# Performance work log

Measured on AMD Instinct MI355X. Metric: run time of the kernel, lower is better.

The kernel has to match this reference:

```python
import jax, jax.numpy as jnp
import numpy as np

EPS = 1e-6
LN3 = 1.0986122886681098  # ternary_softmax uses base-3 exponentials: 3**x / sum(3**x)
ROPE_BASE = 10000.0


def exact_rmsnorm(x, g):
    # ExactRMSNorm: x / sqrt(mean(x^2) + eps) * g
    ms = jnp.mean(jnp.square(x), axis=-1, keepdims=True)
    return x * jax.lax.rsqrt(ms + EPS) * g


def ternary_rope(t):
    # Rotary embedding whose cos/sin tables are quantized to {-1, 0, +1}
    # (round() of cos/sin in [-1,1] yields exactly the ternary set).
    S, D = t.shape[-2], t.shape[-1]
    half = D // 2
    inv_freq = 1.0 / (ROPE_BASE ** (jnp.arange(half, dtype=jnp.float32) / half))
    ang = jnp.arange(S, dtype=jnp.float32)[:, None] * inv_freq[None, :]  # [S, half]
    cos = jnp.round(jnp.cos(ang))
    sin = jnp.round(jnp.sin(ang))
    cos = jnp.concatenate([cos, cos], axis=-1)  # [S, D]
    sin = jnp.concatenate([sin, sin], axis=-1)
    rot = jnp.concatenate([-t[..., half:], t[..., :half]], axis=-1)
    return t * cos + rot * sin


def ternary_softmax(x, axis=-1):
    # softmax in base 3: 3**x / sum(3**x) == softmax(x * ln 3)
    return jax.nn.softmax(x * LN3, axis=axis)


def setup_inputs() -> dict:
    key = jax.random.key(0)
    ks = jax.random.split(key, 6)
    B, S, D = 4, 4096, 1024
    x = jax.random.normal(ks[0], (B, S, D), dtype=jnp.float32)
    g_norm = jnp.ones((D,), dtype=jnp.float32)
    w_qkv = jax.random.normal(ks[1], (D, 3 * D), dtype=jnp.float32) * 0.02
    b_qkv = jnp.zeros((3 * D,), dtype=jnp.float32)
    w_proj = jax.random.normal(ks[2], (D, D), dtype=jnp.float32) * 0.02
    b_proj = jnp.zeros((D,), dtype=jnp.float32)
    return {"x": x, "g_norm": g_norm, "w_qkv": w_qkv, "b_qkv": b_qkv,
            "w_proj": w_proj, "b_proj": b_proj}


def reference(x, g_norm, w_qkv, b_qkv, w_proj, b_proj):
    D = x.shape[-1]
    scale = 1.0 / jnp.sqrt(jnp.float32(D))
    residual = x
    h = exact_rmsnorm(x, g_norm)
    qkv = h @ w_qkv + b_qkv  # [B, S, 3D]
    q, k, v = jnp.split(qkv, 3, axis=-1)
    q = ternary_rope(q)
    k = ternary_rope(k)
    scores = jnp.einsum("bsd,btd->bst", q, k) * scale  # [B, S, S]
    attn = ternary_softmax(scores, axis=-1)
    o = jnp.einsum("bst,btd->bsd", attn, v)
    return o @ w_proj + b_proj + residual
```

## Files before the change

### kernel.cpp

```cpp
#include <hip/hip_runtime.h>
#include <hip/hip_fp8.h>
#include <stdint.h>

#define DEVI __device__ __forceinline__

typedef unsigned short u16;
typedef uint8_t u8;
typedef __attribute__((ext_vector_type(8))) __bf16 bf16x8;
typedef __attribute__((ext_vector_type(4))) float f32x4;
typedef __attribute__((ext_vector_type(4))) int i32x4;
typedef __attribute__((ext_vector_type(8))) int i32x8;

DEVI float b2f(u16 u) { union { unsigned int i; float f; } v; v.i = ((unsigned int)u) << 16; return v.f; }
DEVI u16 f2b(float f) {
  union { float f; unsigned int i; } v; v.f = f;
  unsigned int r = v.i + 0x7fffu + ((v.i >> 16) & 1u);
  return (u16)(r >> 16);
}
DEVI u8 f2f8(float f) { __hip_fp8_e4m3 t(f); return t.__x; }

DEVI void gld_lds16(const void* g, void* l) {
  __builtin_amdgcn_global_load_lds((const __attribute__((address_space(1))) unsigned int*)g,
                                   (__attribute__((address_space(3))) unsigned int*)l, 16, 0, 0);
}

DEVI i32x8 ld32(const u8* p0, const u8* p1) {
  i32x4 lo = *(const i32x4*)p0;
  i32x4 hi = *(const i32x4*)p1;
  return __builtin_shufflevector(lo, hi, 0, 1, 2, 3, 4, 5, 6, 7);
}


__global__ __launch_bounds__(256) void k_rmsnorm(const float* __restrict__ x,
                                                 const float* __restrict__ g,
                                                 u8* __restrict__ h) {
  const int row = blockIdx.x;
  const int t = threadIdx.x;
  const float4 v = ((const float4*)(x + (size_t)row * 1024))[t];
  float ss = v.x * v.x + v.y * v.y + v.z * v.z + v.w * v.w;
  for (int off = 32; off > 0; off >>= 1) ss += __shfl_down(ss, off);
  __shared__ float red[4];
  if ((t & 63) == 0) red[t >> 6] = ss;
  __syncthreads();
  const float tot = red[0] + red[1] + red[2] + red[3];
  const float sc = rsqrtf(tot * (1.0f / 1024.0f) + 1e-6f);
  const float4 gv = ((const float4*)g)[t];
  uchar4 o;
  o.x = f2f8(v.x * sc * gv.x); o.y = f2f8(v.y * sc * gv.y);
  o.z = f2f8(v.z * sc * gv.z); o.w = f2f8(v.w * sc * gv.w);
  *(uchar4*)(h + (size_t)row * 1024 + t * 4) = o;
}

__global__ __launch_bounds__(256) void k_transpose_cast(const float* __restrict__ src,
                                                        int rows, int cols,
                                                        u16* __restrict__ dst) {
  __shared__ float tile[32][33];
  const int c0 = blockIdx.x * 32, r0 = blockIdx.y * 32;
  const int tx = threadIdx.x, ty = threadIdx.y;
  for (int i = 0; i < 32; i += 8)
    tile[ty + i][tx] = src[(size_t)(r0 + ty + i) * cols + c0 + tx];
  __syncthreads();
  for (int i = 0; i < 32; i += 8)
    dst[(size_t)(c0 + ty + i) * rows + r0 + tx] = f2b(tile[tx][ty + i]);
}

__global__ __launch_bounds__(256) void k_transpose_cast_f8(const float* __restrict__ src,
                                                           int rows, int cols,
                                                           u8* __restrict__ dst) {
  __shared__ float tile[32][33];
  const int c0 = blockIdx.x * 32, r0 = blockIdx.y * 32;
  const int tx = threadIdx.x, ty = threadIdx.y;
  for (int i = 0; i < 32; i += 8)
    tile[ty + i][tx] = src[(size_t)(r0 + ty + i) * cols + c0 + tx];
  __syncthreads();
  for (int i = 0; i < 32; i += 8)
    dst[(size_t)(c0 + ty + i) * rows + r0 + tx] = f2f8(tile[tx][ty + i] * 32.0f);
}

__global__ __launch_bounds__(256) void k_rope_cast(const u16* __restrict__ q16, const u16* __restrict__ k16,
                                                   u8* __restrict__ q8, u8* __restrict__ k8) {
  const int row = blockIdx.x;
  const int pos = row & 4095;
  const int t = threadIdx.x;
  const int j0 = t * 2;
  float c[2], s[2];
#pragma unroll
  for (int u = 0; u < 2; u++) {
    const float e = (float)(j0 + u) * (1.0f / 512.0f);
    const float invf = exp2f(-13.287712379549449f * e);
    const float ang = (float)pos * invf;
    c[u] = rintf(cosf(ang));
    s[u] = rintf(sinf(ang));
  }
  const u16* qr = q16 + (size_t)row * 1024;
  const u16* kr = k16 + (size_t)row * 1024;
  u8* qo = q8 + (size_t)row * 1024;
  u8* ko = k8 + (size_t)row * 1024;
  const ushort2 qa = *(const ushort2*)(qr + j0), qb = *(const ushort2*)(qr + j0 + 512);
  const ushort2 ka = *(const ushort2*)(kr + j0), kb = *(const ushort2*)(kr + j0 + 512);
  uchar2 o;
  o.x = f2f8(b2f(qa.x) * c[0] - b2f(qb.x) * s[0]);
  o.y = f2f8(b2f(qa.y) * c[1] - b2f(qb.y) * s[1]);
  *(uchar2*)(qo + j0) = o;
  o.x = f2f8(b2f(qb.x) * c[0] + b2f(qa.x) * s[0]);
  o.y = f2f8(b2f(qb.y) * c[1] + b2f(qa.y) * s[1]);
  *(uchar2*)(qo + j0 + 512) = o;
  o.x = f2f8(b2f(ka.x) * c[0] - b2f(kb.x) * s[0]);
  o.y = f2f8(b2f(ka.y) * c[1] - b2f(kb.y) * s[1]);
  *(uchar2*)(ko + j0) = o;
  o.x = f2f8(b2f(kb.x) * c[0] + b2f(ka.x) * s[0]);
  o.y = f2f8(b2f(kb.y) * c[1] + b2f(ka.y) * s[1]);
  *(uchar2*)(ko + j0 + 512) = o;
}

__global__ __launch_bounds__(256) void k_vt(const u16* __restrict__ v, u8* __restrict__ vt) {
  __shared__ u16 tile[32][33];
  const int b = blockIdx.z;
  const int s0 = blockIdx.x * 32, d0 = blockIdx.y * 32;
  const int tx = threadIdx.x, ty = threadIdx.y;
  for (int i = 0; i < 32; i += 8)
    tile[ty + i][tx] = v[(size_t)(b * 4096 + s0 + ty + i) * 1024 + d0 + tx];
  __syncthreads();
  for (int i = 0; i < 32; i += 8)
    vt[(size_t)(b * 1024 + d0 + ty + i) * 4096 + s0 + tx] = f2f8(b2f(tile[tx][ty + i]));
}

DEVI void gemm_tile(const u16* __restrict__ A, int lda,
                    const u16* __restrict__ B, int ldb,
                    int K, int m0, int n0,
                    u16* As, u16* Bs, f32x4 acc[4][4]) {
  const int t = threadIdx.x;
  const int sr = t >> 2;
  const int sc = (t & 3) * 8;
  const u16* Ag0 = A + (size_t)(m0 + sr) * lda + sc;
  const u16* Ag1 = A + (size_t)(m0 + 64 + sr) * lda + sc;
  const u16* Bg0 = B + (size_t)(n0 + sr) * ldb + sc;
  const u16* Bg1 = B + (size_t)(n0 + 64 + sr) * ldb + sc;
  u16* Asw = As + t * 8;
  u16* Bsw = Bs + t * 8;

  const int lane = t & 63, qd = lane >> 4, l16 = lane & 15;
  const int wave = t >> 6;
  const int wm = (wave >> 1) * 64, wn = (wave & 1) * 64;
  const int aoff = (wm + l16) * 32 + qd * 8;
  const int boff = (wn + l16) * 32 + qd * 8;

  auto stage = [&](int sel, int k0) {
    u16* Ad = Asw + sel * 4096;
    u16* Bd = Bsw + sel * 4096;
    gld_lds16(Ag0 + k0, Ad);
    gld_lds16(Ag1 + k0, Ad + 2048);
    gld_lds16(Bg0 + k0, Bd);
    gld_lds16(Bg1 + k0, Bd + 2048);
  };

  stage(0, 0);
  int cur = 0;
  for (int k0 = 0; k0 < K; k0 += 32) {
    if (k0 + 32 < K) {
      stage(cur ^ 1, k0 + 32);
      asm volatile("s_waitcnt vmcnt(4)" ::: "memory");
    } else {
      asm volatile("s_waitcnt vmcnt(0)" ::: "memory");
    }
    __builtin_amdgcn_s_barrier();
    const u16* Ard = As + cur * 4096 + aoff;
    const u16* Brd = Bs + cur * 4096 + boff;
    bf16x8 af[4], bfv[4];
#pragma unroll
    for (int i = 0; i < 4; i++) af[i] = *(const bf16x8*)(Ard + i * 16 * 32);
#pragma unroll
    for (int j = 0; j < 4; j++) bfv[j] = *(const bf16x8*)(Brd + j * 16 * 32);
#pragma unroll
    for (int i = 0; i < 4; i++)
#pragma unroll
      for (int j = 0; j < 4; j++)
        acc[i][j] = __builtin_amdgcn_mfma_f32_16x16x32_bf16(af[i], bfv[j], acc[i][j], 0, 0, 0);
    __builtin_amdgcn_s_barrier();
    cur ^= 1;
  }
}

DEVI void gemm_tile_mx(const u8* __restrict__ A, int lda,
                       const u8* __restrict__ B, int ldb,
                       int K, int m0, int n0,
                       u8* As, u8* Bs, f32x4 acc[4][4], int sB) {
  const int t = threadIdx.x;
  const int sr = t >> 3;
  const int sc = ((t & 7) ^ (sr & 7)) << 4;
  const u8* Agb = A + (size_t)(m0 + sr) * lda + sc;
  const u8* Bgb = B + (size_t)(n0 + sr) * ldb + sc;
  u8* Asw = As + t * 16;
  u8* Bsw = Bs + t * 16;

  const int lane = t & 63, qd = lane >> 4, l16 = lane & 15;
  const int wave = t >> 6;
  const int wm = (wave >> 1) * 64, wn = (wave & 1) * 64;
  const int key = l16 & 7;
  const int c0 = ((qd << 1) ^ key) << 4;
  const int aoff = (wm + l16) * 128 + c0;
  const int boff = (wn + l16) * 128 + c0;

  auto stage = [&](int sel, int k0) {
    u8* Ad = Asw + sel * 16384;
    u8* Bd = Bsw + sel * 16384;
#pragma unroll
    for (int l = 0; l < 4; l++) {
      gld_lds16(Agb + k0 + (size_t)l * 32 * lda, Ad + l * 4096);
      gld_lds16(Bgb + k0 + (size_t)l * 32 * ldb, Bd + l * 4096);
    }
  };

  stage(0, 0);
  int cur = 0;
  for (int k0 = 0; k0 < K; k0 += 128) {
    if (k0 + 128 < K) {
      stage(cur ^ 1, k0 + 128);
      asm volatile("s_waitcnt vmcnt(8)" ::: "memory");
    } else {
      asm volatile("s_waitcnt vmcnt(0)" ::: "memory");
    }
    __builtin_amdgcn_s_barrier();
    const u8* Ab = As + cur * 16384;
    const u8* Bb = Bs + cur * 16384;
    i32x8 a[4], b[4];
#pragma unroll
    for (int i = 0; i < 4; i++)
      a[i] = ld32(Ab + aoff + i * 2048, Ab + (aoff ^ 16) + i * 2048);
#pragma unroll
    for (int j = 0; j < 4; j++)
      b[j] = ld32(Bb + boff + j * 2048, Bb + (boff ^ 16) + j * 2048);
#pragma unroll
    for (int i = 0; i < 4; i++)
#pragma unroll
      for (int j = 0; j < 4; j++)
        acc[i][j] = __builtin_amdgcn_mfma_scale_f32_16x16x128_f8f6f4(
            a[i], b[j], acc[i][j], 0 , 0 ,
            0, 0x7f7f7f7f, 0, sB);
    __builtin_amdgcn_s_barrier();
    cur ^= 1;
  }
}

#define ACC_INIT()                                               \
  f32x4 acc[4][4];                                               \
  _Pragma("unroll") for (int i = 0; i < 4; i++)                  \
      _Pragma("unroll") for (int j = 0; j < 4; j++)              \
          acc[i][j] = f32x4{0.f, 0.f, 0.f, 0.f};

#define GEMM_EPI_IDX()                                           \
  const int t = threadIdx.x, lane = t & 63, qd = lane >> 4,      \
            l16 = lane & 15, wave = t >> 6;                      \
  const int wm = (wave >> 1) * 64, wn = (wave & 1) * 64;         \
  (void)t;


__global__ __launch_bounds__(256) void k_gemm_qkv(const u8* __restrict__ A, const u8* __restrict__ Bt,
                                                  const float* __restrict__ bias,
                                                  u16* __restrict__ q16, u16* __restrict__ k16,
                                                  u16* __restrict__ v16) {
  __shared__ alignas(16) u8 As[32768], Bs[32768];
  ACC_INIT();
  const int m0 = blockIdx.y * 128, n0 = blockIdx.x * 128;
  gemm_tile_mx(A, 1024, Bt, 1024, 1024, m0, n0, As, Bs, acc, 0x7a7a7a7a);
  GEMM_EPI_IDX();
  const int sec = n0 >> 10;
  u16* dst = (sec == 0) ? q16 : (sec == 1) ? k16 : v16;
  const int nb0 = n0 & 1023;
#pragma unroll
  for (int i = 0; i < 4; i++) {
    const int mb = m0 + wm + i * 16 + qd * 4;
#pragma unroll
    for (int j = 0; j < 4; j++) {
      const int col = n0 + wn + j * 16 + l16;
      const float bv = bias[col];
      const int dcol = nb0 + wn + j * 16 + l16;
#pragma unroll
      for (int r = 0; r < 4; r++)
        dst[(size_t)(mb + r) * 1024 + dcol] = f2b(acc[i][j][r] + bv);
    }
  }
}

__global__ __launch_bounds__(256) void k_gemm_scores(const u8* __restrict__ q, const u8* __restrict__ kk,
                                                     u8* __restrict__ P, float* __restrict__ ls) {
  __shared__ alignas(16) u8 As[32768], Bs[32768];
  ACC_INIT();
  const int b = blockIdx.z;
  const u8* A = q + (size_t)b * 4096 * 1024;
  const u8* Bt = kk + (size_t)b * 4096 * 1024;
  const int bid = blockIdx.y * 32 + blockIdx.x;
  const int xcd = bid & 7, idx = bid >> 3;
  const int m0 = ((xcd >> 2) * 16 + (idx & 15)) * 128;
  const int n0 = ((xcd & 3) * 8 + (idx >> 4)) * 128;
  gemm_tile_mx(A, 1024, Bt, 1024, 1024, m0, n0, As, Bs, acc, 0x7f7f7f7f);
  GEMM_EPI_IDX();
  const float C3 = 0.04953007814753613f;
  const size_t Pb = (size_t)b * 4096 * 4096;
  f32x4 rowp[4];
#pragma unroll
  for (int i = 0; i < 4; i++) rowp[i] = f32x4{0.f, 0.f, 0.f, 0.f};
#pragma unroll
  for (int i = 0; i < 4; i++) {
    const int mb = m0 + wm + i * 16 + qd * 4;
#pragma unroll
    for (int j = 0; j < 4; j++) {
      const int col = n0 + wn + j * 16 + l16;
#pragma unroll
      for (int r = 0; r < 4; r++) {
        const float pv = __builtin_amdgcn_exp2f(acc[i][j][r] * C3);
        P[Pb + (size_t)(mb + r) * 4096 + col] = f2f8(pv);
        rowp[i][r] += pv;
      }
    }
  }
#pragma unroll
  for (int m = 1; m < 16; m <<= 1)
#pragma unroll
    for (int i = 0; i < 4; i++) {
      rowp[i].x += __shfl_xor(rowp[i].x, m);
      rowp[i].y += __shfl_xor(rowp[i].y, m);
      rowp[i].z += __shfl_xor(rowp[i].z, m);
      rowp[i].w += __shfl_xor(rowp[i].w, m);
    }
  if (l16 == 0) {
#pragma unroll
    for (int i = 0; i < 4; i++) {
      const int mb = m0 + wm + i * 16 + qd * 4;
#pragma unroll
      for (int r = 0; r < 4; r++)
        atomicAdd(ls + (size_t)b * 4096 + mb + r, rowp[i][r]);
    }
  }
}

__global__ __launch_bounds__(256) void k_gemm_pv(const u8* __restrict__ P, const u8* __restrict__ vt,
                                                 const float* __restrict__ ls, u16* __restrict__ o) {
  __shared__ alignas(16) u8 As[32768], Bs[32768];
  ACC_INIT();
  const int b = blockIdx.z;
  const u8* A = P + (size_t)b * 4096 * 4096;
  const u8* Bt = vt + (size_t)b * 1024 * 4096;
  const int bid = blockIdx.y * 8 + blockIdx.x;
  const int xcd = bid & 7, idx = bid >> 3;
  const int m0 = ((xcd >> 1) * 8 + (idx & 7)) * 128;
  const int n0 = ((xcd & 1) * 4 + (idx >> 3)) * 128;
  gemm_tile_mx(A, 4096, Bt, 4096, 4096, m0, n0, As, Bs, acc, 0x7f7f7f7f);
  GEMM_EPI_IDX();
#pragma unroll
  for (int i = 0; i < 4; i++) {
    const int mb = m0 + wm + i * 16 + qd * 4;
    f32x4 inv;
#pragma unroll
    for (int r = 0; r < 4; r++) inv[r] = 1.0f / ls[(size_t)b * 4096 + mb + r];
#pragma unroll
    for (int j = 0; j < 4; j++) {
      const int col = n0 + wn + j * 16 + l16;
#pragma unroll
      for (int r = 0; r < 4; r++)
        o[(size_t)(b * 4096 + mb + r) * 1024 + col] = f2b(acc[i][j][r] * inv[r]);
    }
  }
}

__global__ __launch_bounds__(256) void k_gemm_proj(const u16* __restrict__ A, const u16* __restrict__ Bt,
                                                   const float* __restrict__ bias, const float* __restrict__ x,
                                                   float* __restrict__ out) {
  __shared__ alignas(16) u16 As[8192], Bs[8192];
  ACC_INIT();
  const int m0 = blockIdx.y * 128, n0 = blockIdx.x * 128;
  gemm_tile(A, 1024, Bt, 1024, 1024, m0, n0, As, Bs, acc);
  GEMM_EPI_IDX();
#pragma unroll
  for (int i = 0; i < 4; i++) {
    const int mb = m0 + wm + i * 16 + qd * 4;
#pragma unroll
    for (int j = 0; j < 4; j++) {
      const int col = n0 + wn + j * 16 + l16;
      const float bv = bias[col];
#pragma unroll
      for (int r = 0; r < 4; r++) {
        const size_t idxo = (size_t)(mb + r) * 1024 + col;
        out[idxo] = acc[i][j][r] + bv + x[idxo];
      }
    }
  }
}

extern "C" void kernel_launch(void* const* d_in, const int* in_sizes, int n_in,
                              void* d_out, int out_size, void* d_ws, size_t ws_size,
                              hipStream_t stream) {
  const float* x     = (const float*)d_in[0];
  const float* g     = (const float*)d_in[1];
  const float* wqkv  = (const float*)d_in[2];
  const float* bqkv  = (const float*)d_in[3];
  const float* wproj = (const float*)d_in[4];
  const float* bproj = (const float*)d_in[5];
  float* out = (float*)d_out;

  char* wsp = (char*)d_ws;
  size_t off = 0;
  auto take = [&](size_t bytes) -> void* {
    off = (off + 255) & ~(size_t)255;
    void* r = wsp + off;
    off += bytes;
    return r;
  };
  char* hreg = (char*)take(16384ull * 1024 * 2);
  u8*  h8   = (u8*)hreg;
  u16* o16  = (u16*)hreg;
  u8*  wqT8 = (u8*)take(3072ull * 1024);
  u16* wpT  = (u16*)take(1024ull * 1024 * 2);
  u8*  q8   = (u8*)take(16384ull * 1024);
  u8*  k8   = (u8*)take(16384ull * 1024);
  u8*  vt   = (u8*)take(4ull * 1024 * 4096);
  float* ls = (float*)take(16384ull * 4);
  char* scratch = (char*)take(3ull * 16384 * 1024 * 2);
  u16* q16 = (u16*)scratch;
  u16* k16 = (u16*)(scratch + 16384ull * 1024 * 2);
  u16* v16 = (u16*)(scratch + 2ull * 16384 * 1024 * 2);
  u8*  P   = (u8*)scratch;

  k_transpose_cast_f8<<<dim3(3072 / 32, 1024 / 32), dim3(32, 8), 0, stream>>>(wqkv, 1024, 3072, wqT8);
  k_transpose_cast<<<dim3(1024 / 32, 1024 / 32), dim3(32, 8), 0, stream>>>(wproj, 1024, 1024, wpT);
  k_rmsnorm<<<16384, 256, 0, stream>>>(x, g, h8);
  k_gemm_qkv<<<dim3(24, 128), 256, 0, stream>>>(h8, wqT8, bqkv, q16, k16, v16);
  k_rope_cast<<<16384, 256, 0, stream>>>(q16, k16, q8, k8);
  k_vt<<<dim3(128, 32, 4), dim3(32, 8), 0, stream>>>(v16, vt);
  hipMemsetAsync(ls, 0, 16384 * 4, stream);
  k_gemm_scores<<<dim3(32, 32, 4), 256, 0, stream>>>(q8, k8, P, ls);
  k_gemm_pv<<<dim3(8, 32, 4), 256, 0, stream>>>(P, vt, ls, o16);
  k_gemm_proj<<<dim3(8, 128), 256, 0, stream>>>(o16, wpT, bproj, x, out);
}
```

Measured before the change: 504.1 us.

## Load FP8 GEMM A operand directly into registers, staging only B through LDS

In the MX-FP8 GEMM tile routine, the A operand is no longer staged through shared memory. Each lane now loads its own A fragment straight from global memory into registers, double-buffered in two register sets, while B keeps its double-buffered LDS staging. The loop is unrolled by two K-steps to alternate the buffers. This halves LDS usage, which may allow more workgroups per CU, and removes LDS write/read traffic for A. In exchange it adds register pressure and less-coalesced direct global loads whose A rows are shared between waves.

After: 655.0 us. 1.3x slower.

```diff
diff --git a/kernel.cpp b/kernel.cpp
--- a/kernel.cpp
+++ b/kernel.cpp
@@ -24,10 +24,11 @@
                                    (__attribute__((address_space(3))) unsigned int*)l, 16, 0, 0);
 }
 
+DEVI i32x8 cat32(i32x4 lo, i32x4 hi) {
+  return __builtin_shufflevector(lo, hi, 0, 1, 2, 3, 4, 5, 6, 7);
+}
 DEVI i32x8 ld32(const u8* p0, const u8* p1) {
-  i32x4 lo = *(const i32x4*)p0;
-  i32x4 hi = *(const i32x4*)p1;
-  return __builtin_shufflevector(lo, hi, 0, 1, 2, 3, 4, 5, 6, 7);
+  return cat32(*(const i32x4*)p0, *(const i32x4*)p1);
 }
 
 
@@ -184,13 +185,11 @@
 DEVI void gemm_tile_mx(const u8* __restrict__ A, int lda,
                        const u8* __restrict__ B, int ldb,
                        int K, int m0, int n0,
-                       u8* As, u8* Bs, f32x4 acc[4][4], int sB) {
+                       u8* Bs, f32x4 acc[4][4], int sB) {
   const int t = threadIdx.x;
   const int sr = t >> 3;
   const int sc = ((t & 7) ^ (sr & 7)) << 4;
-  const u8* Agb = A + (size_t)(m0 + sr) * lda + sc;
   const u8* Bgb = B + (size_t)(n0 + sr) * ldb + sc;
-  u8* Asw = As + t * 16;
   u8* Bsw = Bs + t * 16;
 
   const int lane = t & 63, qd = lane >> 4, l16 = lane & 15;
@@ -198,47 +197,60 @@
   const int wm = (wave >> 1) * 64, wn = (wave & 1) * 64;
   const int key = l16 & 7;
   const int c0 = ((qd << 1) ^ key) << 4;
-  const int aoff = (wm + l16) * 128 + c0;
   const int boff = (wn + l16) * 128 + c0;
 
-  auto stage = [&](int sel, int k0) {
-    u8* Ad = Asw + sel * 16384;
+  const u8* Ab = A + (size_t)(m0 + wm + l16) * lda + qd * 32;
+
+  auto stageB = [&](int sel, int k0) {
     u8* Bd = Bsw + sel * 16384;
 #pragma unroll
-    for (int l = 0; l < 4; l++) {
-      gld_lds16(Agb + k0 + (size_t)l * 32 * lda, Ad + l * 4096);
+    for (int l = 0; l < 4; l++)
       gld_lds16(Bgb + k0 + (size_t)l * 32 * ldb, Bd + l * 4096);
-    }
   };
-
-  stage(0, 0);
-  int cur = 0;
-  for (int k0 = 0; k0 < K; k0 += 128) {
-    if (k0 + 128 < K) {
-      stage(cur ^ 1, k0 + 128);
-      asm volatile("s_waitcnt vmcnt(8)" ::: "memory");
+  auto loadA = [&](int k0, i32x4* ax) {
+#pragma unroll
+    for (int i = 0; i < 4; i++) {
+      const u8* p = Ab + (size_t)i * 16 * lda + k0;
+      ax[2 * i]     = *(const i32x4*)p;
+      ax[2 * i + 1] = *(const i32x4*)(p + 16);
+    }
+  };
+  auto compute = [&](const u8* Bb, const i32x4* ax) {
+    i32x8 b[4];
+#pragma unroll
+    for (int j = 0; j < 4; j++)
+      b[j] = ld32(Bb + boff + j * 2048, Bb + (boff ^ 16) + j * 2048);
+#pragma unroll
+    for (int i = 0; i < 4; i++) {
+      const i32x8 a = cat32(ax[2 * i], ax[2 * i + 1]);
+#pragma unroll
+      for (int j = 0; j < 4; j++)
+        acc[i][j] = __builtin_amdgcn_mfma_scale_f32_16x16x128_f8f6f4(
+            a, b[j], acc[i][j], 0 , 0 ,
+            0, 0x7f7f7f7f, 0, sB);
+    }
+  };
+
+  i32x4 aX[8], aY[8];
+  loadA(0, aX);
+  stageB(0, 0);
+  for (int k0 = 0; k0 < K; k0 += 256) {
+    loadA(k0 + 128, aY);
+    stageB(1, k0 + 128);
+    asm volatile("s_waitcnt vmcnt(12)" ::: "memory");
+    __builtin_amdgcn_s_barrier();
+    compute(Bs, aX);
+    __builtin_amdgcn_s_barrier();
+    if (k0 + 256 < K) {
+      loadA(k0 + 256, aX);
+      stageB(0, k0 + 256);
+      asm volatile("s_waitcnt vmcnt(12)" ::: "memory");
     } else {
       asm volatile("s_waitcnt vmcnt(0)" ::: "memory");
     }
     __builtin_amdgcn_s_barrier();
-    const u8* Ab = As + cur * 16384;
-    const u8* Bb = Bs + cur * 16384;
-    i32x8 a[4], b[4];
-#pragma unroll
-    for (int i = 0; i < 4; i++)
-      a[i] = ld32(Ab + aoff + i * 2048, Ab + (aoff ^ 16) + i * 2048);
-#pragma unroll
-    for (int j = 0; j < 4; j++)
-      b[j] = ld32(Bb + boff + j * 2048, Bb + (boff ^ 16) + j * 2048);
-#pragma unroll
-    for (int i = 0; i < 4; i++)
-#pragma unroll
-      for (int j = 0; j < 4; j++)
-        acc[i][j] = __builtin_amdgcn_mfma_scale_f32_16x16x128_f8f6f4(
-            a[i], b[j], acc[i][j], 0 , 0 ,
-            0, 0x7f7f7f7f, 0, sB);
-    __builtin_amdgcn_s_barrier();
-    cur ^= 1;
+    compute(Bs + 16384, aY);
+    __builtin_amdgcn_s_barrier();
   }
 }
 
@@ -259,10 +271,10 @@
                                                   const float* __restrict__ bias,
                                                   u16* __restrict__ q16, u16* __restrict__ k16,
                                                   u16* __restrict__ v16) {
-  __shared__ alignas(16) u8 As[32768], Bs[32768];
+  __shared__ alignas(16) u8 Bs[32768];
   ACC_INIT();
   const int m0 = blockIdx.y * 128, n0 = blockIdx.x * 128;
-  gemm_tile_mx(A, 1024, Bt, 1024, 1024, m0, n0, As, Bs, acc, 0x7a7a7a7a);
+  gemm_tile_mx(A, 1024, Bt, 1024, 1024, m0, n0, Bs, acc, 0x7a7a7a7a);
   GEMM_EPI_IDX();
   const int sec = n0 >> 10;
   u16* dst = (sec == 0) ? q16 : (sec == 1) ? k16 : v16;
@@ -284,7 +296,7 @@
 
 __global__ __launch_bounds__(256) void k_gemm_scores(const u8* __restrict__ q, const u8* __restrict__ kk,
                                                      u8* __restrict__ P, float* __restrict__ ls) {
-  __shared__ alignas(16) u8 As[32768], Bs[32768];
+  __shared__ alignas(16) u8 Bs[32768];
   ACC_INIT();
   const int b = blockIdx.z;
   const u8* A = q + (size_t)b * 4096 * 1024;
@@ -293,7 +305,7 @@
   const int xcd = bid & 7, idx = bid >> 3;
   const int m0 = ((xcd >> 2) * 16 + (idx & 15)) * 128;
   const int n0 = ((xcd & 3) * 8 + (idx >> 4)) * 128;
-  gemm_tile_mx(A, 1024, Bt, 1024, 1024, m0, n0, As, Bs, acc, 0x7f7f7f7f);
+  gemm_tile_mx(A, 1024, Bt, 1024, 1024, m0, n0, Bs, acc, 0x7f7f7f7f);
   GEMM_EPI_IDX();
   const float C3 = 0.04953007814753613f;
   const size_t Pb = (size_t)b * 4096 * 4096;
@@ -336,7 +348,7 @@
 
 __global__ __launch_bounds__(256) void k_gemm_pv(const u8* __restrict__ P, const u8* __restrict__ vt,
                                                  const float* __restrict__ ls, u16* __restrict__ o) {
-  __shared__ alignas(16) u8 As[32768], Bs[32768];
+  __shared__ alignas(16) u8 Bs[32768];
   ACC_INIT();
   const int b = blockIdx.z;
   const u8* A = P + (size_t)b * 4096 * 4096;
@@ -345,7 +357,7 @@
   const int xcd = bid & 7, idx = bid >> 3;
   const int m0 = ((xcd >> 1) * 8 + (idx & 7)) * 128;
   const int n0 = ((xcd & 1) * 4 + (idx >> 3)) * 128;
-  gemm_tile_mx(A, 4096, Bt, 4096, 4096, m0, n0, As, Bs, acc, 0x7f7f7f7f);
+  gemm_tile_mx(A, 4096, Bt, 4096, 4096, m0, n0, Bs, acc, 0x7f7f7f7f);
   GEMM_EPI_IDX();
 #pragma unroll
   for (int i = 0; i < 4; i++) {
```

## Fuse V transpose and fp8 cast into QKV GEMM epilogue; raise MFMA priority

Applied to the files above, without the earlier changes.

The QKV GEMM epilogue now writes the V section directly as a transposed fp8 tensor, staging the tile in shared memory. This removes the separate k_vt kernel and the bf16 round trip of V through global memory. The GEMM inner loops also raise wave priority with s_setprio around the MFMA blocks. The costs are extra LDS staging and a __syncthreads in the V-section blocks, plus a possible bank-conflict penalty from the 144-byte stride.

Result: faster. 456.2 us, median of 2 (-9.5%).

```diff
diff --git a/kernel.cpp b/kernel.cpp
--- a/kernel.cpp
+++ b/kernel.cpp
@@ -113,18 +113,6 @@
   *(uchar2*)(ko + j0 + 512) = o;
 }
 
-__global__ __launch_bounds__(256) void k_vt(const u16* __restrict__ v, u8* __restrict__ vt) {
-  __shared__ u16 tile[32][33];
-  const int b = blockIdx.z;
-  const int s0 = blockIdx.x * 32, d0 = blockIdx.y * 32;
-  const int tx = threadIdx.x, ty = threadIdx.y;
-  for (int i = 0; i < 32; i += 8)
-    tile[ty + i][tx] = v[(size_t)(b * 4096 + s0 + ty + i) * 1024 + d0 + tx];
-  __syncthreads();
-  for (int i = 0; i < 32; i += 8)
-    vt[(size_t)(b * 1024 + d0 + ty + i) * 4096 + s0 + tx] = f2f8(b2f(tile[tx][ty + i]));
-}
-
 DEVI void gemm_tile(const u16* __restrict__ A, int lda,
                     const u16* __restrict__ B, int ldb,
                     int K, int m0, int n0,
@@ -171,11 +159,13 @@
     for (int i = 0; i < 4; i++) af[i] = *(const bf16x8*)(Ard + i * 16 * 32);
 #pragma unroll
     for (int j = 0; j < 4; j++) bfv[j] = *(const bf16x8*)(Brd + j * 16 * 32);
+    __builtin_amdgcn_s_setprio(1);
 #pragma unroll
     for (int i = 0; i < 4; i++)
 #pragma unroll
       for (int j = 0; j < 4; j++)
         acc[i][j] = __builtin_amdgcn_mfma_f32_16x16x32_bf16(af[i], bfv[j], acc[i][j], 0, 0, 0);
+    __builtin_amdgcn_s_setprio(0);
     __builtin_amdgcn_s_barrier();
     cur ^= 1;
   }
@@ -230,6 +220,7 @@
 #pragma unroll
     for (int j = 0; j < 4; j++)
       b[j] = ld32(Bb + boff + j * 2048, Bb + (boff ^ 16) + j * 2048);
+    __builtin_amdgcn_s_setprio(1);
 #pragma unroll
     for (int i = 0; i < 4; i++)
 #pragma unroll
@@ -237,6 +228,7 @@
         acc[i][j] = __builtin_amdgcn_mfma_scale_f32_16x16x128_f8f6f4(
             a[i], b[j], acc[i][j], 0 , 0 ,
             0, 0x7f7f7f7f, 0, sB);
+    __builtin_amdgcn_s_setprio(0);
     __builtin_amdgcn_s_barrier();
     cur ^= 1;
   }
@@ -258,27 +250,52 @@
 __global__ __launch_bounds__(256) void k_gemm_qkv(const u8* __restrict__ A, const u8* __restrict__ Bt,
                                                   const float* __restrict__ bias,
                                                   u16* __restrict__ q16, u16* __restrict__ k16,
-                                                  u16* __restrict__ v16) {
+                                                  u8* __restrict__ vt) {
   __shared__ alignas(16) u8 As[32768], Bs[32768];
   ACC_INIT();
   const int m0 = blockIdx.y * 128, n0 = blockIdx.x * 128;
   gemm_tile_mx(A, 1024, Bt, 1024, 1024, m0, n0, As, Bs, acc, 0x7a7a7a7a);
   GEMM_EPI_IDX();
   const int sec = n0 >> 10;
-  u16* dst = (sec == 0) ? q16 : (sec == 1) ? k16 : v16;
   const int nb0 = n0 & 1023;
-#pragma unroll
-  for (int i = 0; i < 4; i++) {
-    const int mb = m0 + wm + i * 16 + qd * 4;
-#pragma unroll
-    for (int j = 0; j < 4; j++) {
-      const int col = n0 + wn + j * 16 + l16;
-      const float bv = bias[col];
-      const int dcol = nb0 + wn + j * 16 + l16;
-#pragma unroll
-      for (int r = 0; r < 4; r++)
-        dst[(size_t)(mb + r) * 1024 + dcol] = f2b(acc[i][j][r] + bv);
-    }
+  if (sec < 2) {
+    u16* dst = (sec == 0) ? q16 : k16;
+#pragma unroll
+    for (int i = 0; i < 4; i++) {
+      const int mb = m0 + wm + i * 16 + qd * 4;
+#pragma unroll
+      for (int j = 0; j < 4; j++) {
+        const int col = n0 + wn + j * 16 + l16;
+        const float bv = bias[col];
+        const int dcol = nb0 + wn + j * 16 + l16;
+#pragma unroll
+        for (int r = 0; r < 4; r++)
+          dst[(size_t)(mb + r) * 1024 + dcol] = f2b(acc[i][j][r] + bv);
+      }
+    }
+  } else {
+    u8* T = As;
+    const int STR = 144;
+#pragma unroll
+    for (int i = 0; i < 4; i++) {
+      const int mloc = wm + i * 16 + qd * 4;
+#pragma unroll
+      for (int j = 0; j < 4; j++) {
+        const int dloc = wn + j * 16 + l16;
+        const float bv = bias[n0 + wn + j * 16 + l16];
+#pragma unroll
+        for (int r = 0; r < 4; r++)
+          T[dloc * STR + mloc + r] = f2f8(acc[i][j][r] + bv);
+      }
+    }
+    __syncthreads();
+    const int b = m0 >> 12;
+    const int s0 = m0 & 4095;
+    const int row = t >> 1, half = (t & 1) * 64;
+    u8* dst = vt + ((size_t)(b * 1024 + nb0 + row)) * 4096 + s0 + half;
+#pragma unroll
+    for (int c = 0; c < 4; c++)
+      *(i32x4*)(dst + c * 16) = *(const i32x4*)(T + row * STR + half + c * 16);
   }
 }
 
@@ -418,15 +435,13 @@
   char* scratch = (char*)take(3ull * 16384 * 1024 * 2);
   u16* q16 = (u16*)scratch;
   u16* k16 = (u16*)(scratch + 16384ull * 1024 * 2);
-  u16* v16 = (u16*)(scratch + 2ull * 16384 * 1024 * 2);
   u8*  P   = (u8*)scratch;
 
   k_transpose_cast_f8<<<dim3(3072 / 32, 1024 / 32), dim3(32, 8), 0, stream>>>(wqkv, 1024, 3072, wqT8);
   k_transpose_cast<<<dim3(1024 / 32, 1024 / 32), dim3(32, 8), 0, stream>>>(wproj, 1024, 1024, wpT);
   k_rmsnorm<<<16384, 256, 0, stream>>>(x, g, h8);
-  k_gemm_qkv<<<dim3(24, 128), 256, 0, stream>>>(h8, wqT8, bqkv, q16, k16, v16);
+  k_gemm_qkv<<<dim3(24, 128), 256, 0, stream>>>(h8, wqT8, bqkv, q16, k16, vt);
   k_rope_cast<<<16384, 256, 0, stream>>>(q16, k16, q8, k8);
-  k_vt<<<dim3(128, 32, 4), dim3(32, 8), 0, stream>>>(v16, vt);
   hipMemsetAsync(ls, 0, 16384 * 4, stream);
   k_gemm_scores<<<dim3(32, 32, 4), 256, 0, stream>>>(q8, k8, P, ls);
   k_gemm_pv<<<dim3(8, 32, 4), 256, 0, stream>>>(P, vt, ls, o16);
```
